# Optimization experiments

Hardware: AMD Instinct MI355X
Metric: run time of the kernel (lower is better)

The kernel has to match this reference:

```python
import jax, jax.numpy as jnp
import numpy as np
from jax import lax

T, B, D_IN, D_DAY, H, D_OUT = 64, 32, 4096, 256, 256, 942


def setup_inputs() -> dict:
    key = jax.random.key(0)
    ks = jax.random.split(key, 18)
    s = 0.05
    def rn(k, shape):
        return jax.random.normal(k, shape, jnp.float32) * s
    return {
        "x": jax.random.uniform(ks[0], (T, B, D_IN), jnp.float32),
        "W_emb": rn(ks[1], (D_DAY, D_IN)), "b_emb": rn(ks[2], (D_DAY,)),
        "Wih_f": rn(ks[3], (3 * H, D_DAY)), "Whh_f": rn(ks[4], (3 * H, H)),
        "bih_f": rn(ks[5], (3 * H,)), "bhh_f": rn(ks[6], (3 * H,)),
        "Wih_r": rn(ks[7], (3 * H, D_DAY)), "Whh_r": rn(ks[8], (3 * H, H)),
        "bih_r": rn(ks[9], (3 * H,)), "bhh_r": rn(ks[10], (3 * H,)),
        "attn_w": rn(ks[11], (2 * H,)), "attn_b": rn(ks[12], ()),
        "W_ao": rn(ks[13], (D_DAY, 4 * H)), "b_ao": rn(ks[14], (D_DAY,)),
        "W_o": rn(ks[15], (D_OUT, D_DAY)), "b_o": rn(ks[16], (D_OUT,)),
    }


def _gru_cell(xt, h, Wih, Whh, bih, bhh):
    # PyTorch nn.GRU cell math
    gi = xt @ Wih.T + bih          # [B, 3H]
    gh = h @ Whh.T + bhh           # [B, 3H]
    ir, iz, inn = jnp.split(gi, 3, axis=-1)
    hr, hz, hn = jnp.split(gh, 3, axis=-1)
    r = jax.nn.sigmoid(ir + hr)
    z = jax.nn.sigmoid(iz + hz)
    n = jnp.tanh(inn + r * hn)
    return (1.0 - z) * n + z * h


def _run_gru(seq, Wih, Whh, bih, bhh):
    # seq: [L, B, D] -> all hidden states [L, B, H], h0 = zeros
    h0 = jnp.zeros((seq.shape[1], H), seq.dtype)
    def step(h, xt):
        h2 = _gru_cell(xt, h, Wih, Whh, bih, bhh)
        return h2, h2
    return lax.scan(step, h0, seq)[1]


def reference(x, W_emb, b_emb, Wih_f, Whh_f, bih_f, bhh_f,
              Wih_r, Whh_r, bih_r, bhh_r, attn_w, attn_b,
              W_ao, b_ao, W_o, b_o):
    day_emb = jnp.einsum('tbi,di->tbd', x, W_emb) + b_emb       # [T,B,Dday]

    # Forward GRU over the prefix [:i+1] equals the first i+1 states of one full run.
    fwd = _run_gru(day_emb, Wih_f, Whh_f, bih_f, bhh_f)          # [T,B,H]

    # Reverse GRU is recomputed per timestep on the flipped prefix (O(T^2)).
    i_idx = jnp.arange(T)
    j_idx = jnp.arange(T)
    gather = jnp.clip(i_idx[:, None] - j_idx[None, :], 0)        # [T,T]
    rev_in = day_emb[gather]                                     # [T,T,B,Dday]; row i, step j = day_emb[i-j]
    rev = jax.vmap(lambda s: _run_gru(s, Wih_r, Whh_r, bih_r, bhh_r))(rev_in)  # [T,T,B,H]

    # Attention scores on concat(fwd, rev) without materializing the 2H concat:
    w_f, w_r = attn_w[:H], attn_w[H:]
    scores = (jnp.einsum('tbh,h->tb', fwd, w_f)[None, :, :]
              + jnp.einsum('itbh,h->itb', rev, w_r) + attn_b)    # [T(i),T(t),B]
    valid = j_idx[None, :] <= i_idx[:, None]                     # t <= i
    scores = jnp.where(valid[:, :, None], scores, -jnp.inf)
    alpha = jax.nn.softmax(scores, axis=1)                       # softmax over prefix time

    counts = (i_idx + 1).astype(day_emb.dtype)[:, None, None]    # mean over i+1 steps
    c_fwd = jnp.einsum('itb,tbh->ibh', alpha, fwd) / counts      # [T,B,H]
    c_rev = jnp.einsum('itb,itbh->ibh', alpha, rev) / counts     # [T,B,H]
    rev_last = rev[i_idx, i_idx]                                 # rnn_h[-1] reverse half, [T,B,H]

    h_t = jnp.concatenate([c_fwd, c_rev, fwd, rev_last], axis=-1)  # [T,B,4H]
    h_t_out = h_t @ W_ao.T + b_ao                                # [T,B,Dday]
    return jax.nn.sigmoid(h_t_out @ W_o.T + b_o)                 # [T,B,D_OUT]
```

## Files before the change

kernel.cpp:

```cpp
#include <hip/hip_runtime.h>
#include <hip/hip_bf16.h>


typedef __bf16 bf16x8 __attribute__((ext_vector_type(8)));
typedef __bf16 bf16x4 __attribute__((ext_vector_type(4)));
typedef float  f32x4  __attribute__((ext_vector_type(4)));
typedef int    int4v  __attribute__((ext_vector_type(4)));

static constexpr float NEG_L2E = -1.442695041f;
static constexpr float TWO_L2E =  2.885390082f;

static constexpr size_t OFF_PK_EMB = 0;
static constexpr size_t OFF_PK_IH  = 2097152;
static constexpr size_t OFF_WQ     = 2883584;
static constexpr size_t OFF_WSC    = 3276800;
static constexpr size_t OFF_PK_AO  = 3670016;
static constexpr size_t OFF_PK_O   = 4194304;
static constexpr size_t OFF_DAY    = 4685824;
static constexpr size_t OFF_GIT    = 5734400;
static constexpr size_t OFF_BC     = 12025856;
static constexpr size_t OFF_REV    = 18317312;
static constexpr size_t OFF_FWD    = 52396032;
static constexpr size_t OFF_HT     = 53444608;
static constexpr size_t OFF_TMP1   = 57638912;
static constexpr size_t OFF_XB     = OFF_REV;

__device__ __forceinline__ float sigf(float x) {
    return __builtin_amdgcn_rcpf(1.f + __expf(-x));
}

#define LDS_BARRIER() asm volatile("s_waitcnt lgkmcnt(0)\n\ts_barrier" ::: "memory")

__global__ __launch_bounds__(256) void pack_misc(
    const float* __restrict__ We,  const float* __restrict__ Wir, const float* __restrict__ Wif,
    const float* __restrict__ Wao, const float* __restrict__ Wo,  const float* __restrict__ x,
    __bf16* pe, __bf16* pi, __bf16* pao, __bf16* po, __bf16* xb)
{
    int b = blockIdx.x;
    if (b >= 952) {
        size_t base = ((size_t)(b - 952) * 256 + threadIdx.x) * 8;
        float4 v0 = *(const float4*)(x + base);
        float4 v1 = *(const float4*)(x + base + 4);
        bf16x8 o;
        o[0]=(__bf16)v0.x; o[1]=(__bf16)v0.y; o[2]=(__bf16)v0.z; o[3]=(__bf16)v0.w;
        o[4]=(__bf16)v1.x; o[5]=(__bf16)v1.y; o[6]=(__bf16)v1.z; o[7]=(__bf16)v1.w;
        *(bf16x8*)(xb + base) = o;
        return;
    }
    const float* src; __bf16* dst; int Nsrc, k32l, b0; bool ih = false;
    if (b < 512)      { src = We;  dst = pe;          Nsrc = 256; k32l = 7; b0 = 0;   }
    else if (b < 608) { src = Wir; dst = pi;          Nsrc = 768; k32l = 3; b0 = 512; ih = true; }
    else if (b < 704) { src = Wif; dst = pi + 196608; Nsrc = 768; k32l = 3; b0 = 608; ih = true; }
    else if (b < 832) { src = Wao; dst = pao;         Nsrc = 256; k32l = 5; b0 = 704; }
    else              { src = Wo;  dst = po;          Nsrc = 942; k32l = 3; b0 = 832; }
    int t8   = (b - b0) * 256 + threadIdx.x;
    int lane = t8 & 63;
    int K32  = 1 << k32l;
    int K    = K32 << 5;
    int ks   = (t8 >> 6) & (K32 - 1);
    int nt   = t8 >> (6 + k32l);
    int n    = nt * 16 + (lane & 15);
    int k0   = ks * 32 + ((lane >> 4) << 3);
    bf16x8 o;
    if (n < Nsrc) {
        const float* sp = src + (size_t)n * K + k0;
        float4 v0 = *(const float4*)sp;
        float4 v1 = *(const float4*)(sp + 4);
        float s = ih ? ((n < 512) ? NEG_L2E : TWO_L2E) : 1.f;
        o[0]=(__bf16)(v0.x*s); o[1]=(__bf16)(v0.y*s); o[2]=(__bf16)(v0.z*s); o[3]=(__bf16)(v0.w*s);
        o[4]=(__bf16)(v1.x*s); o[5]=(__bf16)(v1.y*s); o[6]=(__bf16)(v1.z*s); o[7]=(__bf16)(v1.w*s);
    } else {
#pragma unroll
        for (int q = 0; q < 8; q++) o[q] = (__bf16)0.f;
    }
    *(bf16x8*)(dst + (size_t)t8 * 8) = o;
}

__global__ __launch_bounds__(64) void pack_hh_i8(
    const float* __restrict__ Whr, const float* __restrict__ Whf,
    const float* __restrict__ bih_r, const float* __restrict__ bih_f,
    const float* __restrict__ bhh_r, const float* __restrict__ bhh_f,
    signed char* __restrict__ wq, float* __restrict__ wscale, float* __restrict__ bc)
{
    int b = blockIdx.x;
    int dir = (b >= 768) ? 1 : 0;
    int n = b - dir * 768;
    const float* src = (dir ? Whf : Whr) + (size_t)n * 256;
    int t = threadIdx.x;
    float4 wv = ((const float4*)src)[t];
    float m = fmaxf(fmaxf(fabsf(wv.x), fabsf(wv.y)), fmaxf(fabsf(wv.z), fabsf(wv.w)));
#pragma unroll
    for (int off = 32; off > 0; off >>= 1) m = fmaxf(m, __shfl_xor(m, off));
    m = fmaxf(m, 1e-20f);
    float inv = 127.f / m;
    int q0 = (int)__builtin_rintf(wv.x * inv);
    int q1 = (int)__builtin_rintf(wv.y * inv);
    int q2 = (int)__builtin_rintf(wv.z * inv);
    int q3 = (int)__builtin_rintf(wv.w * inv);
    int pk = (q0 & 0xff) | ((q1 & 0xff) << 8) | ((q2 & 0xff) << 16) | ((q3 & 0xff) << 24);
    int dlane = (n & 15) | (((t >> 2) & 3) << 4);
    size_t byte = (size_t)dir * 196608 + ((size_t)(n >> 4) * 4 + (t >> 4)) * 1024
                + (size_t)dlane * 16 + (t & 3) * 4;
    *(int*)(wq + byte) = pk;
    if (t == 0) {
        float gc = (n < 512) ? NEG_L2E : TWO_L2E;
        wscale[b] = m * (1.f / 16129.f) * gc;
        const float* bi = dir ? bih_f : bih_r;
        const float* bh = dir ? bhh_f : bhh_r;
        bc[b] = (n < 512) ? (bi[n] + bh[n]) * NEG_L2E : bi[n] * TWO_L2E;
    }
}

template<int MODE, int KDIM, int NTILES, int MR, int CSTRIDE, int NREAL>
__global__ __launch_bounds__(256) void gemm_k(
    const __bf16* __restrict__ Ap, const __bf16* __restrict__ Bp, void* __restrict__ Cp,
    const float* __restrict__ bias)
{
    __shared__ __align__(16) __bf16 As[MR][88];
    const int tid = threadIdx.x;
    const int w = tid >> 6, lane = tid & 63, c = lane & 15, quad = lane >> 4;
    const int mb = blockIdx.x, nb = blockIdx.y;
    constexpr int K32 = KDIM / 32;
    constexpr int NK  = KDIM / 64;
    constexpr int NT_W = (MR == 64) ? NTILES : NTILES / 2;
    constexpr int TPR  = (MR == 64) ? 4 : 8;
    constexpr int EPT  = 64 / TPR;
    const int wrow  = (MR == 64) ? w : (w & 1);
    const int ncol0 = (MR == 64) ? 0 : (w >> 1) * NT_W;

    f32x4 acc[NT_W];
#pragma unroll
    for (int nt = 0; nt < NT_W; nt++) acc[nt] = (f32x4){0.f, 0.f, 0.f, 0.f};

    const int row = tid / TPR, kp = (tid % TPR) * EPT;
    uint4 pb[EPT / 8];

    auto issue = [&](int kb) {
        const __bf16* ap = Ap + (size_t)(mb * MR + row) * KDIM + kb * 64 + kp;
        pb[0] = ((const uint4*)ap)[0];
        if constexpr (EPT == 16) pb[1] = ((const uint4*)ap)[1];
    };
    auto commit = [&]() {
        *(uint4*)&As[row][kp] = pb[0];
        if constexpr (EPT == 16) *(uint4*)&As[row][kp + 8] = pb[1];
    };

    issue(0);
    for (int kb = 0; kb < NK; kb++) {
        commit();
        __syncthreads();
        if (kb + 1 < NK) issue(kb + 1);
#pragma unroll
        for (int kk = 0; kk < 2; kk++) {
            bf16x8 a = *(const bf16x8*)&As[wrow * 16 + c][kk * 32 + quad * 8];
#pragma unroll
            for (int nt = 0; nt < NT_W; nt++) {
                bf16x8 bfr = *(const bf16x8*)(Bp +
                    ((size_t)((nb * NTILES + ncol0 + nt) * K32 + kb * 2 + kk) * 64 + lane) * 8);
                acc[nt] = __builtin_amdgcn_mfma_f32_16x16x32_bf16(a, bfr, acc[nt], 0, 0, 0);
            }
        }
        __syncthreads();
    }

    if constexpr (MODE == 1) {
        static_assert(MR == 64 && NTILES == 4, "MODE1 epilogue requires 64x64 tile");
#pragma unroll
        for (int nt = 0; nt < 4; nt++) {
            float bv = bias[nb * 64 + nt * 16 + c];
#pragma unroll
            for (int r0 = 0; r0 < 4; r0++)
                As[nt * 16 + c][w * 16 + quad * 4 + r0] = (__bf16)(acc[nt][r0] + bv);
        }
        __syncthreads();
        const int dd = tid >> 2, bch = tid & 3;
        const int n = nb * 64 + dd;
        const int dir = (n >= 768) ? 1 : 0;
        const int rem = n - dir * 768;
        const int g = rem >> 8, dcol = rem & 255;
#pragma unroll
        for (int tl = 0; tl < 2; tl++) {
            uint4 v = *(const uint4*)&As[dd][tl * 32 + bch * 8];
            size_t off = (size_t)dir * 1572864 + (size_t)(mb * 2 + tl) * 24576
                       + ((size_t)((g * 2 + (bch >> 1)) * 256 + dcol)) * 16 + (bch & 1) * 8;
            *(uint4*)((__bf16*)Cp + off) = v;
        }
    } else {
#pragma unroll
        for (int nt = 0; nt < NT_W; nt++) {
            int n = nb * (NTILES * 16) + (ncol0 + nt) * 16 + c;
            float bv = (n < NREAL) ? bias[n] : 0.f;
#pragma unroll
            for (int r0 = 0; r0 < 4; r0++) {
                int m = mb * MR + wrow * 16 + quad * 4 + r0;
                float v = acc[nt][r0] + bv;
                if constexpr (MODE == 2) ((__bf16*)Cp)[(size_t)m * CSTRIDE + n] = (__bf16)v;
                else { if (n < NREAL) ((float*)Cp)[(size_t)m * CSTRIDE + n] = sigf(v); }
            }
        }
    }
}

__global__ __launch_bounds__(1024, 4) void gru_recurrent(
    const signed char* __restrict__ wq, const float* __restrict__ wscale,
    const float* __restrict__ bhh_r, const float* __restrict__ bhh_f,
    const __bf16* __restrict__ Git,
    __bf16* __restrict__ revb, __bf16* __restrict__ fwdb)
{
    __shared__ __align__(16) signed char hbuf[2][16][272];
    __shared__ __align__(16) __bf16 hist[8][4096];
    const int tid = threadIdx.x;
    const int w = tid >> 6, lane = tid & 63, c = lane & 15, quad = lane >> 4;
    const int bid = blockIdx.x;
    const bool isF = (bid < 2);
    const int ia = isF ? 63 : (63 - ((bid - 2) >> 1));
    const int bh = bid & 1;
    const int b0 = bh << 4;
    const int steps = ia + 1;
    const float* bhh = isF ? bhh_f : bhh_r;
    __bf16* outb = isF ? fwdb : (revb + ((size_t)(ia * (ia + 1) / 2)) * 8192);

    const int4v* pw = (const int4v*)(wq + (isF ? 196608 : 0));
    int4v bw[3][4];
#pragma unroll
    for (int g = 0; g < 3; g++)
#pragma unroll
        for (int ks = 0; ks < 4; ks++)
            bw[g][ks] = pw[(size_t)((g * 16 + w) * 4 + ks) * 64 + lane];
    const int d = (w << 4) + c;
    float sc[3];
#pragma unroll
    for (int g = 0; g < 3; g++) sc[g] = wscale[(isF ? 768 : 0) + g * 256 + d];
    const float bnv = bhh[512 + d] * TWO_L2E;

    float hreg[4] = {0.f, 0.f, 0.f, 0.f};
    for (int idx = tid; idx < 2 * 16 * 272 / 4; idx += 1024) ((int*)hbuf)[idx] = 0;
    __syncthreads();

    const __bf16* gb = Git + (size_t)(isF ? 64 : ia) * 24576;
    const long gstep = isF ? 24576 : -24576;
    int loff[3];
#pragma unroll
    for (int g = 0; g < 3; g++) loff[g] = ((g * 2 + bh) * 256 + d) * 16 + (quad << 2);

    auto flush = [&](int jbase, int cnt) {
        int s = tid >> 7;
        if (s < cnt) {
            const uint4* src = (const uint4*)((const char*)&hist[s][0] + (tid & 127) * 64);
            uint4 v0 = src[0], v1 = src[1], v2 = src[2], v3 = src[3];
            uint4* dst = (uint4*)(outb + (size_t)(jbase + s) * 8192 + b0 * 256 + (tid & 127) * 32);
            dst[0] = v0; dst[1] = v1; dst[2] = v2; dst[3] = v3;
        }
    };

    bf16x4 gcur[3], gnxt[3];
#pragma unroll
    for (int g = 0; g < 3; g++) gcur[g] = *(const bf16x4*)(gb + loff[g]);

    for (int j = 0; j < steps; j++) {
        const int rb = j & 1, wbuf = rb ^ 1;

        if (j + 1 < steps) {
            const __bf16* gn = gb + gstep;
#pragma unroll
            for (int g = 0; g < 3; g++) gnxt[g] = *(const bf16x4*)(gn + loff[g]);
        }

        int4v a0 = {0,0,0,0}, a1 = {0,0,0,0}, a2 = {0,0,0,0};
#pragma unroll
        for (int ks = 0; ks < 4; ks++) {
            int4v av = *(const int4v*)&hbuf[rb][c][ks * 64 + quad * 16];
            a0 = __builtin_amdgcn_mfma_i32_16x16x64_i8(av, bw[0][ks], a0, 0, 0, 0);
            a1 = __builtin_amdgcn_mfma_i32_16x16x64_i8(av, bw[1][ks], a1, 0, 0, 0);
            a2 = __builtin_amdgcn_mfma_i32_16x16x64_i8(av, bw[2][ks], a2, 0, 0, 0);
        }

        const int hs = j & 7;
#pragma unroll
        for (int r0 = 0; r0 < 4; r0++) {
            float er = __builtin_amdgcn_exp2f(fmaf((float)a0[r0], sc[0], (float)gcur[0][r0]));
            float rg = __builtin_amdgcn_rcpf(1.f + er);
            float ez = __builtin_amdgcn_exp2f(fmaf((float)a1[r0], sc[1], (float)gcur[1][r0]));
            float zg = __builtin_amdgcn_rcpf(1.f + ez);
            float narg = fmaf(rg, fmaf((float)a2[r0], sc[2], bnv), (float)gcur[2][r0]);
            float en = __builtin_amdgcn_exp2f(narg);
            float ng = fmaf(-2.f, __builtin_amdgcn_rcpf(1.f + en), 1.f);
            float h  = fmaf(zg, hreg[r0] - ng, ng);
            hreg[r0] = h;
            int row = (quad << 2) + r0;
            hbuf[wbuf][row][d] = (signed char)(int)__builtin_rintf(h * 127.f);
            hist[hs][row * 256 + d] = (__bf16)h;
        }
        LDS_BARRIER();
        if (hs == 7) {
            flush(j - 7, 8);
            LDS_BARRIER();
        }
        gb += gstep;
#pragma unroll
        for (int g = 0; g < 3; g++) gcur[g] = gnxt[g];
    }
    int rem = steps & 7;
    if (rem) flush(steps - rem, rem);
}

__global__ __launch_bounds__(512) void attn_kernel(
    const __bf16* __restrict__ revb, const __bf16* __restrict__ fwdb,
    const float* __restrict__ attn_w, const float* __restrict__ attn_bp,
    __bf16* __restrict__ ht)
{
    const int tid = threadIdx.x;
    const int w = tid >> 6, lane = tid & 63;
    const int wid = blockIdx.x * 8 + w;
    const int i = wid >> 5, b = wid & 31;
    const int d0 = lane * 4;

    float wf[4], wr[4];
#pragma unroll
    for (int q = 0; q < 4; q++) { wf[q] = attn_w[d0 + q]; wr[q] = attn_w[256 + d0 + q]; }
    const float ab = attn_bp[0];
    const __bf16* rp = revb + ((size_t)(i * (i + 1) / 2)) * 8192 + (size_t)b * 256 + d0;
    const __bf16* fp = fwdb + (size_t)b * 256 + d0;

    float mx = -1e30f, l = 0.f;
    float cf[4] = {0,0,0,0}, cr[4] = {0,0,0,0};
    bf16x4 rn = *(const bf16x4*)rp, fn = *(const bf16x4*)fp;
    for (int t = 0; t <= i; t++) {
        bf16x4 rv4 = rn, fv4 = fn;
        if (t < i) {
            rn = *(const bf16x4*)(rp + (size_t)(t + 1) * 8192);
            fn = *(const bf16x4*)(fp + (size_t)(t + 1) * 8192);
        }
        float rv[4], fv[4], s = 0.f;
#pragma unroll
        for (int q = 0; q < 4; q++) {
            rv[q] = (float)rv4[q]; fv[q] = (float)fv4[q];
            s += rv[q] * wr[q] + fv[q] * wf[q];
        }
#pragma unroll
        for (int off = 32; off > 0; off >>= 1) s += __shfl_xor(s, off);
        s += ab;
        float mn = fmaxf(mx, s);
        float scl = __expf(mx - mn);
        float p  = __expf(s - mn);
        l = l * scl + p;
#pragma unroll
        for (int q = 0; q < 4; q++) { cf[q] = cf[q] * scl + p * fv[q]; cr[q] = cr[q] * scl + p * rv[q]; }
        mx = mn;
    }
    float inv = __builtin_amdgcn_rcpf(l * (float)(i + 1));
    __bf16* hp = ht + (size_t)(i * 32 + b) * 1024 + d0;
    const __bf16* fl = fp + (size_t)i * 8192;
    const __bf16* rl = rp + (size_t)i * 8192;
#pragma unroll
    for (int q = 0; q < 4; q++) {
        hp[q]       = (__bf16)(cf[q] * inv);
        hp[256 + q] = (__bf16)(cr[q] * inv);
        hp[512 + q] = fl[q];
        hp[768 + q] = rl[q];
    }
}

extern "C" void kernel_launch(void* const* d_in, const int* in_sizes, int n_in,
                              void* d_out, int out_size, void* d_ws, size_t ws_size,
                              hipStream_t stream) {
    const float* x      = (const float*)d_in[0];
    const float* W_emb  = (const float*)d_in[1];
    const float* b_emb  = (const float*)d_in[2];
    const float* Wih_f  = (const float*)d_in[3];
    const float* Whh_f  = (const float*)d_in[4];
    const float* bih_f  = (const float*)d_in[5];
    const float* bhh_f  = (const float*)d_in[6];
    const float* Wih_r  = (const float*)d_in[7];
    const float* Whh_r  = (const float*)d_in[8];
    const float* bih_r  = (const float*)d_in[9];
    const float* bhh_r  = (const float*)d_in[10];
    const float* attn_w = (const float*)d_in[11];
    const float* attn_b = (const float*)d_in[12];
    const float* W_ao   = (const float*)d_in[13];
    const float* b_ao   = (const float*)d_in[14];
    const float* W_o    = (const float*)d_in[15];
    const float* b_o    = (const float*)d_in[16];
    float* out = (float*)d_out;

    char* ws = (char*)d_ws;
    __bf16* pk_emb = (__bf16*)(ws + OFF_PK_EMB);
    __bf16* pk_ih  = (__bf16*)(ws + OFF_PK_IH);
    signed char* wq = (signed char*)(ws + OFF_WQ);
    float*  wsc    = (float*)(ws + OFF_WSC);
    __bf16* pk_ao  = (__bf16*)(ws + OFF_PK_AO);
    __bf16* pk_o   = (__bf16*)(ws + OFF_PK_O);
    __bf16* day    = (__bf16*)(ws + OFF_DAY);
    __bf16* Git    = (__bf16*)(ws + OFF_GIT);
    float*  bc     = (float*)(ws + OFF_BC);
    __bf16* revb   = (__bf16*)(ws + OFF_REV);
    __bf16* fwdb   = (__bf16*)(ws + OFF_FWD);
    __bf16* ht     = (__bf16*)(ws + OFF_HT);
    __bf16* tmp1   = (__bf16*)(ws + OFF_TMP1);
    __bf16* xb     = (__bf16*)(ws + OFF_XB);

    pack_misc<<<5048, 256, 0, stream>>>(W_emb, Wih_r, Wih_f, W_ao, W_o, x,
                                        pk_emb, pk_ih, pk_ao, pk_o, xb);
    pack_hh_i8<<<1536, 64, 0, stream>>>(Whh_r, Whh_f, bih_r, bih_f, bhh_r, bhh_f,
                                        wq, wsc, bc);

    gemm_k<2, 4096, 4, 32, 256, 256><<<dim3(64, 4), 256, 0, stream>>>(xb, pk_emb, day, b_emb);
    gemm_k<1, 256, 4, 64, 1536, 1536><<<dim3(32, 24), 256, 0, stream>>>(day, pk_ih, Git, bc);

    gru_recurrent<<<130, 1024, 0, stream>>>(wq, wsc, bhh_r, bhh_f, Git, revb, fwdb);

    attn_kernel<<<256, 512, 0, stream>>>(revb, fwdb, attn_w, attn_b, ht);

    gemm_k<2, 1024, 4, 32, 256, 256><<<dim3(64, 4), 256, 0, stream>>>(ht, pk_ao, tmp1, b_ao);
    gemm_k<3, 256, 4, 32, 942, 942><<<dim3(64, 15), 256, 0, stream>>>(tmp1, pk_o, out, b_o);
}
```

Measured before the change: 350.0 us.

## Restructure GRU recurrence to 512 threads with row-major gate inputs and direct stores

The GRU recurrent kernel now runs 512 threads per block, each wave covering two 16-column tiles. It reads input gate projections from a plain row-major [T*B,1536] buffer and writes hidden states straight to global memory every step instead of staging 8 steps in LDS and flushing. The special permuted-layout GEMM epilogue is dropped, and the GEMM now prefetches B fragments one k-block ahead. This trades less LDS and fewer barriers for more per-thread register work and smaller, more scattered global stores per step.

New measurement: 350.0 us. About the same (-0.0%).

```diff
diff --git a/kernel.cpp b/kernel.cpp
--- a/kernel.cpp
+++ b/kernel.cpp
@@ -111,197 +111,195 @@
     }
 }
 
-template<int MODE, int KDIM, int NTILES, int MR, int CSTRIDE, int NREAL>
+template<int MODE, int KDIM, int NTILES, int CSTRIDE, int NREAL>
 __global__ __launch_bounds__(256) void gemm_k(
     const __bf16* __restrict__ Ap, const __bf16* __restrict__ Bp, void* __restrict__ Cp,
     const float* __restrict__ bias)
 {
-    __shared__ __align__(16) __bf16 As[MR][88];
+    __shared__ __align__(16) __bf16 As[32][88];
     const int tid = threadIdx.x;
     const int w = tid >> 6, lane = tid & 63, c = lane & 15, quad = lane >> 4;
     const int mb = blockIdx.x, nb = blockIdx.y;
     constexpr int K32 = KDIM / 32;
     constexpr int NK  = KDIM / 64;
-    constexpr int NT_W = (MR == 64) ? NTILES : NTILES / 2;
-    constexpr int TPR  = (MR == 64) ? 4 : 8;
-    constexpr int EPT  = 64 / TPR;
-    const int wrow  = (MR == 64) ? w : (w & 1);
-    const int ncol0 = (MR == 64) ? 0 : (w >> 1) * NT_W;
+    constexpr int NT_W = NTILES / 2;
+    const int wrow = w & 1, ncol0 = (w >> 1) * NT_W;
 
     f32x4 acc[NT_W];
 #pragma unroll
     for (int nt = 0; nt < NT_W; nt++) acc[nt] = (f32x4){0.f, 0.f, 0.f, 0.f};
 
-    const int row = tid / TPR, kp = (tid % TPR) * EPT;
-    uint4 pb[EPT / 8];
-
-    auto issue = [&](int kb) {
-        const __bf16* ap = Ap + (size_t)(mb * MR + row) * KDIM + kb * 64 + kp;
-        pb[0] = ((const uint4*)ap)[0];
-        if constexpr (EPT == 16) pb[1] = ((const uint4*)ap)[1];
+    const int row = tid >> 3, kp = (tid & 7) * 8;
+    uint4 pb;
+    auto issue  = [&](int kb) { pb = *(const uint4*)(Ap + (size_t)(mb * 32 + row) * KDIM + kb * 64 + kp); };
+    auto commit = [&]() { *(uint4*)&As[row][kp] = pb; };
+
+    bf16x8 bcur[2][NT_W], bnxt[2][NT_W];
+    auto loadB = [&](int kb, bf16x8 (&dst)[2][NT_W]) {
+#pragma unroll
+        for (int kk = 0; kk < 2; kk++)
+#pragma unroll
+            for (int nt = 0; nt < NT_W; nt++)
+                dst[kk][nt] = *(const bf16x8*)(Bp +
+                    ((size_t)((nb * NTILES + ncol0 + nt) * K32 + kb * 2 + kk) * 64 + lane) * 8);
     };
-    auto commit = [&]() {
-        *(uint4*)&As[row][kp] = pb[0];
-        if constexpr (EPT == 16) *(uint4*)&As[row][kp + 8] = pb[1];
-    };
 
     issue(0);
+    loadB(0, bcur);
     for (int kb = 0; kb < NK; kb++) {
         commit();
         __syncthreads();
-        if (kb + 1 < NK) issue(kb + 1);
+        if (kb + 1 < NK) { issue(kb + 1); loadB(kb + 1, bnxt); }
 #pragma unroll
         for (int kk = 0; kk < 2; kk++) {
             bf16x8 a = *(const bf16x8*)&As[wrow * 16 + c][kk * 32 + quad * 8];
 #pragma unroll
-            for (int nt = 0; nt < NT_W; nt++) {
-                bf16x8 bfr = *(const bf16x8*)(Bp +
-                    ((size_t)((nb * NTILES + ncol0 + nt) * K32 + kb * 2 + kk) * 64 + lane) * 8);
-                acc[nt] = __builtin_amdgcn_mfma_f32_16x16x32_bf16(a, bfr, acc[nt], 0, 0, 0);
-            }
+            for (int nt = 0; nt < NT_W; nt++)
+                acc[nt] = __builtin_amdgcn_mfma_f32_16x16x32_bf16(a, bcur[kk][nt], acc[nt], 0, 0, 0);
+        }
+        if (kb + 1 < NK) {
+#pragma unroll
+            for (int kk = 0; kk < 2; kk++)
+#pragma unroll
+                for (int nt = 0; nt < NT_W; nt++) bcur[kk][nt] = bnxt[kk][nt];
         }
         __syncthreads();
     }
 
-    if constexpr (MODE == 1) {
-        static_assert(MR == 64 && NTILES == 4, "MODE1 epilogue requires 64x64 tile");
-#pragma unroll
-        for (int nt = 0; nt < 4; nt++) {
-            float bv = bias[nb * 64 + nt * 16 + c];
-#pragma unroll
-            for (int r0 = 0; r0 < 4; r0++)
-                As[nt * 16 + c][w * 16 + quad * 4 + r0] = (__bf16)(acc[nt][r0] + bv);
-        }
-        __syncthreads();
-        const int dd = tid >> 2, bch = tid & 3;
-        const int n = nb * 64 + dd;
-        const int dir = (n >= 768) ? 1 : 0;
-        const int rem = n - dir * 768;
-        const int g = rem >> 8, dcol = rem & 255;
-#pragma unroll
-        for (int tl = 0; tl < 2; tl++) {
-            uint4 v = *(const uint4*)&As[dd][tl * 32 + bch * 8];
-            size_t off = (size_t)dir * 1572864 + (size_t)(mb * 2 + tl) * 24576
-                       + ((size_t)((g * 2 + (bch >> 1)) * 256 + dcol)) * 16 + (bch & 1) * 8;
-            *(uint4*)((__bf16*)Cp + off) = v;
-        }
-    } else {
-#pragma unroll
-        for (int nt = 0; nt < NT_W; nt++) {
-            int n = nb * (NTILES * 16) + (ncol0 + nt) * 16 + c;
-            float bv = (n < NREAL) ? bias[n] : 0.f;
-#pragma unroll
-            for (int r0 = 0; r0 < 4; r0++) {
-                int m = mb * MR + wrow * 16 + quad * 4 + r0;
-                float v = acc[nt][r0] + bv;
-                if constexpr (MODE == 2) ((__bf16*)Cp)[(size_t)m * CSTRIDE + n] = (__bf16)v;
-                else { if (n < NREAL) ((float*)Cp)[(size_t)m * CSTRIDE + n] = sigf(v); }
-            }
-        }
-    }
-}
-
-__global__ __launch_bounds__(1024, 4) void gru_recurrent(
+#pragma unroll
+    for (int nt = 0; nt < NT_W; nt++) {
+        int n = nb * (NTILES * 16) + (ncol0 + nt) * 16 + c;
+        float bv = (n < NREAL) ? bias[n] : 0.f;
+#pragma unroll
+        for (int r0 = 0; r0 < 4; r0++) {
+            int m = mb * 32 + wrow * 16 + quad * 4 + r0;
+            float v = acc[nt][r0] + bv;
+            if constexpr (MODE == 0) ((__bf16*)Cp)[(size_t)m * CSTRIDE + n] = (__bf16)v;
+            else { if (n < NREAL) ((float*)Cp)[(size_t)m * CSTRIDE + n] = sigf(v); }
+        }
+    }
+}
+
+__global__ __launch_bounds__(512, 2) void gru_recurrent(
     const signed char* __restrict__ wq, const float* __restrict__ wscale,
     const float* __restrict__ bhh_r, const float* __restrict__ bhh_f,
-    const __bf16* __restrict__ Git,
+    const __bf16* __restrict__ Gi,
     __bf16* __restrict__ revb, __bf16* __restrict__ fwdb)
 {
     __shared__ __align__(16) signed char hbuf[2][16][272];
-    __shared__ __align__(16) __bf16 hist[8][4096];
     const int tid = threadIdx.x;
     const int w = tid >> 6, lane = tid & 63, c = lane & 15, quad = lane >> 4;
     const int bid = blockIdx.x;
     const bool isF = (bid < 2);
     const int ia = isF ? 63 : (63 - ((bid - 2) >> 1));
-    const int bh = bid & 1;
-    const int b0 = bh << 4;
+    const int b0 = (bid & 1) << 4;
     const int steps = ia + 1;
     const float* bhh = isF ? bhh_f : bhh_r;
     __bf16* outb = isF ? fwdb : (revb + ((size_t)(ia * (ia + 1) / 2)) * 8192);
+    const int dirb = isF ? 768 : 0;
 
     const int4v* pw = (const int4v*)(wq + (isF ? 196608 : 0));
-    int4v bw[3][4];
+    int4v bw[3][2][4];
 #pragma unroll
     for (int g = 0; g < 3; g++)
 #pragma unroll
-        for (int ks = 0; ks < 4; ks++)
-            bw[g][ks] = pw[(size_t)((g * 16 + w) * 4 + ks) * 64 + lane];
-    const int d = (w << 4) + c;
-    float sc[3];
-#pragma unroll
-    for (int g = 0; g < 3; g++) sc[g] = wscale[(isF ? 768 : 0) + g * 256 + d];
-    const float bnv = bhh[512 + d] * TWO_L2E;
-
-    float hreg[4] = {0.f, 0.f, 0.f, 0.f};
-    for (int idx = tid; idx < 2 * 16 * 272 / 4; idx += 1024) ((int*)hbuf)[idx] = 0;
+        for (int tl = 0; tl < 2; tl++)
+#pragma unroll
+            for (int ks = 0; ks < 4; ks++)
+                bw[g][tl][ks] = pw[(size_t)((g * 16 + 2 * w + tl) * 4 + ks) * 64 + lane];
+
+    const int d0q = (w << 5) + (quad << 2);
+    f32x4 sc[3][2], bnv[2];
+#pragma unroll
+    for (int g = 0; g < 3; g++)
+#pragma unroll
+        for (int tl = 0; tl < 2; tl++)
+            sc[g][tl] = *(const f32x4*)&wscale[dirb + g * 256 + d0q + tl * 16];
+#pragma unroll
+    for (int tl = 0; tl < 2; tl++) {
+        f32x4 bv = *(const f32x4*)&bhh[512 + d0q + tl * 16];
+#pragma unroll
+        for (int q = 0; q < 4; q++) bnv[tl][q] = bv[q] * TWO_L2E;
+    }
+
+    float hreg[2][4] = {{0,0,0,0},{0,0,0,0}};
+    for (int idx = tid; idx < 2 * 16 * 272 / 4; idx += 512) ((int*)hbuf)[idx] = 0;
     __syncthreads();
 
-    const __bf16* gb = Git + (size_t)(isF ? 64 : ia) * 24576;
-    const long gstep = isF ? 24576 : -24576;
-    int loff[3];
-#pragma unroll
-    for (int g = 0; g < 3; g++) loff[g] = ((g * 2 + bh) * 256 + d) * 16 + (quad << 2);
-
-    auto flush = [&](int jbase, int cnt) {
-        int s = tid >> 7;
-        if (s < cnt) {
-            const uint4* src = (const uint4*)((const char*)&hist[s][0] + (tid & 127) * 64);
-            uint4 v0 = src[0], v1 = src[1], v2 = src[2], v3 = src[3];
-            uint4* dst = (uint4*)(outb + (size_t)(jbase + s) * 8192 + b0 * 256 + (tid & 127) * 32);
-            dst[0] = v0; dst[1] = v1; dst[2] = v2; dst[3] = v3;
-        }
-    };
-
-    bf16x4 gcur[3], gnxt[3];
-#pragma unroll
-    for (int g = 0; g < 3; g++) gcur[g] = *(const bf16x4*)(gb + loff[g]);
+    const __bf16* grow = Gi + ((size_t)((isF ? 0 : ia) * 32 + b0 + c)) * 1536 + dirb + d0q;
+    const long gstep = isF ? (32 * 1536) : -(32 * 1536);
+    __bf16* go = outb + (size_t)(b0 + c) * 256 + d0q;
+
+    bf16x4 gcur[3][2], gnxt[3][2];
+#pragma unroll
+    for (int g = 0; g < 3; g++)
+#pragma unroll
+        for (int tl = 0; tl < 2; tl++)
+            gcur[g][tl] = *(const bf16x4*)(grow + g * 256 + tl * 16);
 
     for (int j = 0; j < steps; j++) {
         const int rb = j & 1, wbuf = rb ^ 1;
-
-        if (j + 1 < steps) {
-            const __bf16* gn = gb + gstep;
-#pragma unroll
-            for (int g = 0; g < 3; g++) gnxt[g] = *(const bf16x4*)(gn + loff[g]);
-        }
-
-        int4v a0 = {0,0,0,0}, a1 = {0,0,0,0}, a2 = {0,0,0,0};
+        const bool more = (j + 1 < steps);
+
+        if (more) {
+            grow += gstep;
+#pragma unroll
+            for (int g = 0; g < 3; g++)
+#pragma unroll
+                for (int tl = 0; tl < 2; tl++)
+                    gnxt[g][tl] = *(const bf16x4*)(grow + g * 256 + tl * 16);
+        }
+
+        int4v acc[3][2];
+#pragma unroll
+        for (int g = 0; g < 3; g++)
+#pragma unroll
+            for (int tl = 0; tl < 2; tl++) acc[g][tl] = (int4v){0, 0, 0, 0};
 #pragma unroll
         for (int ks = 0; ks < 4; ks++) {
-            int4v av = *(const int4v*)&hbuf[rb][c][ks * 64 + quad * 16];
-            a0 = __builtin_amdgcn_mfma_i32_16x16x64_i8(av, bw[0][ks], a0, 0, 0, 0);
-            a1 = __builtin_amdgcn_mfma_i32_16x16x64_i8(av, bw[1][ks], a1, 0, 0, 0);
-            a2 = __builtin_amdgcn_mfma_i32_16x16x64_i8(av, bw[2][ks], a2, 0, 0, 0);
-        }
-
-        const int hs = j & 7;
-#pragma unroll
-        for (int r0 = 0; r0 < 4; r0++) {
-            float er = __builtin_amdgcn_exp2f(fmaf((float)a0[r0], sc[0], (float)gcur[0][r0]));
-            float rg = __builtin_amdgcn_rcpf(1.f + er);
-            float ez = __builtin_amdgcn_exp2f(fmaf((float)a1[r0], sc[1], (float)gcur[1][r0]));
-            float zg = __builtin_amdgcn_rcpf(1.f + ez);
-            float narg = fmaf(rg, fmaf((float)a2[r0], sc[2], bnv), (float)gcur[2][r0]);
-            float en = __builtin_amdgcn_exp2f(narg);
-            float ng = fmaf(-2.f, __builtin_amdgcn_rcpf(1.f + en), 1.f);
-            float h  = fmaf(zg, hreg[r0] - ng, ng);
-            hreg[r0] = h;
-            int row = (quad << 2) + r0;
-            hbuf[wbuf][row][d] = (signed char)(int)__builtin_rintf(h * 127.f);
-            hist[hs][row * 256 + d] = (__bf16)h;
-        }
+            int4v av = *(const int4v*)&hbuf[rb][c][ks * 64 + (quad << 4)];
+#pragma unroll
+            for (int g = 0; g < 3; g++)
+#pragma unroll
+                for (int tl = 0; tl < 2; tl++)
+                    acc[g][tl] = __builtin_amdgcn_mfma_i32_16x16x64_i8(bw[g][tl][ks], av,
+                                                                       acc[g][tl], 0, 0, 0);
+        }
+
+#pragma unroll
+        for (int tl = 0; tl < 2; tl++) {
+            int pk = 0;
+            bf16x4 hb;
+#pragma unroll
+            for (int r0 = 0; r0 < 4; r0++) {
+                float er = __builtin_amdgcn_exp2f(fmaf((float)acc[0][tl][r0], sc[0][tl][r0],
+                                                       (float)gcur[0][tl][r0]));
+                float rg = __builtin_amdgcn_rcpf(1.f + er);
+                float ez = __builtin_amdgcn_exp2f(fmaf((float)acc[1][tl][r0], sc[1][tl][r0],
+                                                       (float)gcur[1][tl][r0]));
+                float zg = __builtin_amdgcn_rcpf(1.f + ez);
+                float narg = fmaf(rg, fmaf((float)acc[2][tl][r0], sc[2][tl][r0], bnv[tl][r0]),
+                                  (float)gcur[2][tl][r0]);
+                float en = __builtin_amdgcn_exp2f(narg);
+                float ng = fmaf(-2.f, __builtin_amdgcn_rcpf(1.f + en), 1.f);
+                float h  = fmaf(zg, hreg[tl][r0] - ng, ng);
+                hreg[tl][r0] = h;
+                int q = (int)__builtin_rintf(h * 127.f);
+                pk |= (q & 0xff) << (8 * r0);
+                hb[r0] = (__bf16)h;
+            }
+            *(int*)&hbuf[wbuf][c][d0q + tl * 16] = pk;
+            *(bf16x4*)(go + tl * 16) = hb;
+        }
+        go += 8192;
         LDS_BARRIER();
-        if (hs == 7) {
-            flush(j - 7, 8);
-            LDS_BARRIER();
-        }
-        gb += gstep;
-#pragma unroll
-        for (int g = 0; g < 3; g++) gcur[g] = gnxt[g];
-    }
-    int rem = steps & 7;
-    if (rem) flush(steps - rem, rem);
+        if (more) {
+#pragma unroll
+            for (int g = 0; g < 3; g++)
+#pragma unroll
+                for (int tl = 0; tl < 2; tl++) gcur[g][tl] = gnxt[g][tl];
+        }
+    }
 }
 
 __global__ __launch_bounds__(512) void attn_kernel(
@@ -391,7 +389,7 @@
     __bf16* pk_ao  = (__bf16*)(ws + OFF_PK_AO);
     __bf16* pk_o   = (__bf16*)(ws + OFF_PK_O);
     __bf16* day    = (__bf16*)(ws + OFF_DAY);
-    __bf16* Git    = (__bf16*)(ws + OFF_GIT);
+    __bf16* Gi     = (__bf16*)(ws + OFF_GIT);
     float*  bc     = (float*)(ws + OFF_BC);
     __bf16* revb   = (__bf16*)(ws + OFF_REV);
     __bf16* fwdb   = (__bf16*)(ws + OFF_FWD);
@@ -404,13 +402,13 @@
     pack_hh_i8<<<1536, 64, 0, stream>>>(Whh_r, Whh_f, bih_r, bih_f, bhh_r, bhh_f,
                                         wq, wsc, bc);
 
-    gemm_k<2, 4096, 4, 32, 256, 256><<<dim3(64, 4), 256, 0, stream>>>(xb, pk_emb, day, b_emb);
-    gemm_k<1, 256, 4, 64, 1536, 1536><<<dim3(32, 24), 256, 0, stream>>>(day, pk_ih, Git, bc);
-
-    gru_recurrent<<<130, 1024, 0, stream>>>(wq, wsc, bhh_r, bhh_f, Git, revb, fwdb);
+    gemm_k<0, 4096, 4, 256, 256><<<dim3(64, 4), 256, 0, stream>>>(xb, pk_emb, day, b_emb);
+    gemm_k<0, 256, 4, 1536, 1536><<<dim3(64, 24), 256, 0, stream>>>(day, pk_ih, Gi, bc);
+
+    gru_recurrent<<<130, 512, 0, stream>>>(wq, wsc, bhh_r, bhh_f, Gi, revb, fwdb);
 
     attn_kernel<<<256, 512, 0, stream>>>(revb, fwdb, attn_w, attn_b, ht);
 
-    gemm_k<2, 1024, 4, 32, 256, 256><<<dim3(64, 4), 256, 0, stream>>>(ht, pk_ao, tmp1, b_ao);
-    gemm_k<3, 256, 4, 32, 942, 942><<<dim3(64, 15), 256, 0, stream>>>(tmp1, pk_o, out, b_o);
-}
+    gemm_k<0, 1024, 4, 256, 256><<<dim3(64, 4), 256, 0, stream>>>(ht, pk_ao, tmp1, b_ao);
+    gemm_k<1, 256, 4, 942, 942><<<dim3(64, 15), 256, 0, stream>>>(tmp1, pk_o, out, b_o);
+}
```
